# Performance work log

Measured on AMD Instinct MI355X. Metric: run time of the kernel, lower is better.

## Reference

```python
import jax, jax.numpy as jnp
import numpy as np

B, T, IN_DIM, H, W = 32, 20, 3, 1, 256
HID = 64
FC1_IN = HID * T * H * W  # 327680
FC1_OUT = 512
OUT_DIM = 3


def setup_inputs() -> dict:
    key = jax.random.key(0)
    ks = jax.random.split(key, 6)
    s = 0.02
    return dict(
        x=jax.random.normal(ks[0], (B, T, IN_DIM, H, W), dtype=jnp.float32),
        conv_w0=jax.random.normal(ks[1], (4 * HID, IN_DIM + HID, 3, 3), dtype=jnp.float32) * s,
        conv_b0=jnp.zeros((4 * HID,), dtype=jnp.float32),
        conv_w1=jax.random.normal(ks[2], (4 * HID, HID + HID, 3, 3), dtype=jnp.float32) * s,
        conv_b1=jnp.zeros((4 * HID,), dtype=jnp.float32),
        fc1_w=jax.random.normal(ks[3], (FC1_OUT, FC1_IN), dtype=jnp.float32) * s,
        fc1_b=jnp.zeros((FC1_OUT,), dtype=jnp.float32),
        fc2_w=jax.random.normal(ks[4], (OUT_DIM, FC1_OUT), dtype=jnp.float32) * s,
        fc2_b=jnp.zeros((OUT_DIM,), dtype=jnp.float32),
    )


def _convlstm_layer(inp, w, b):
    # inp: (B, T, C, H, W); w: (4*hid, C+hid, kh, kw)
    Bn, Tn, C, Hn, Wn = inp.shape
    hid = w.shape[0] // 4
    h0 = jnp.zeros((Bn, hid, Hn, Wn), inp.dtype)

    def step(carry, x_t):
        h, c = carry
        z = jnp.concatenate([x_t, h], axis=1)  # (B, C+hid, H, W)
        gates = jax.lax.conv_general_dilated(
            z, w, window_strides=(1, 1), padding='SAME',
            dimension_numbers=('NCHW', 'OIHW', 'NCHW')) + b[None, :, None, None]
        i, f, o, g = jnp.split(gates, 4, axis=1)
        c_new = jax.nn.sigmoid(f) * c + jax.nn.sigmoid(i) * jnp.tanh(g)
        h_new = jax.nn.sigmoid(o) * jnp.tanh(c_new)
        return (h_new, c_new), h_new

    _, hs = jax.lax.scan(step, (h0, h0), jnp.swapaxes(inp, 0, 1))
    return jnp.swapaxes(hs, 0, 1)  # (B, T, hid, H, W)


def reference(x, conv_w0, conv_b0, conv_w1, conv_b1, fc1_w, fc1_b, fc2_w, fc2_b):
    h = _convlstm_layer(x, conv_w0, conv_b0)
    h = _convlstm_layer(h, conv_w1, conv_b1)
    flat = h.reshape(h.shape[0], -1)  # (B, T*hid*H*W), torch .view order
    z = jax.nn.relu(flat @ fc1_w.T + fc1_b)
    out = z @ fc2_w.T + fc2_b
    return jnp.concatenate([out[:, :2], jax.nn.sigmoid(out[:, 2:])], axis=1)
```

## Files before the change

### kernel.cpp

```cpp
#include <hip/hip_runtime.h>
#include <hip/hip_bf16.h>
#include <cstddef>

#define BATCH 32
#define TSTEPS 20
#define IN_DIM 3
#define WIDTH 256
#define HID 64
#define FC1_IN 327680
#define FC1_OUT 512
#define OUT_DIM 3

#define CST 5
#define MARG 6
#define REGC 44
#define CORE 6
#define ROWS 50
#define CROWS 48

#define KSLICE 1280
#define KPHASE 640
#define NSPLIT 256

typedef _Float16 half8 __attribute__((ext_vector_type(8)));
typedef float floatx4 __attribute__((ext_vector_type(4)));

__device__ __forceinline__ float sigm(float x) {
    return 1.0f / (1.0f + __expf(-x));
}
__device__ __forceinline__ float tanh_fast(float x) {
    return 1.0f - 2.0f / (__expf(2.0f * x) + 1.0f);
}


__global__ __launch_bounds__(256) void prep_w0(
    const float* __restrict__ cw0, _Float16* __restrict__ wt0)
{
    int e = blockIdx.x * 256 + threadIdx.x;
    if (e >= 256 * 96) return;
    int co = e / 96, cip = e - co * 96;
    int ci = (cip < 64) ? (3 + cip) : (cip < 67 ? cip - 64 : -1);
    float v[3] = {0.f, 0.f, 0.f};
    if (ci >= 0) {
#pragma unroll
        for (int kw = 0; kw < 3; ++kw)
            v[kw] = cw0[(size_t)(co * 67 + ci) * 9 + 3 + kw];
    }
#pragma unroll
    for (int kw = 0; kw < 3; ++kw)
        wt0[(size_t)(kw * 256 + co) * 96 + cip] = (_Float16)v[kw];
}

__global__ __launch_bounds__(256) void prep_w1(
    const float* __restrict__ cw1, _Float16* __restrict__ wt1)
{
    int e = blockIdx.x * 256 + threadIdx.x;
    int co = e >> 7, ci = e & 127;
#pragma unroll
    for (int kw = 0; kw < 3; ++kw)
        wt1[(size_t)(kw * 256 + co) * 128 + ci] =
            (_Float16)cw1[(size_t)(co * 128 + ci) * 9 + 3 + kw];
}

__global__ __launch_bounds__(256) void prep_x(
    const float* __restrict__ x, _Float16* __restrict__ xT)
{
    int e = blockIdx.x * 256 + threadIdx.x;
    if (e >= TSTEPS * BATCH * WIDTH) return;
    int t = e / (BATCH * WIDTH);
    int rem = e - t * BATCH * WIDTH;
    int b = rem >> 8, w = rem & 255;
    half8 v = {};
#pragma unroll
    for (int ci = 0; ci < 3; ++ci)
        v[ci] = (_Float16)x[(size_t)((b * TSTEPS + t) * IN_DIM + ci) * WIDTH + w];
    *(half8*)&xT[(size_t)e * 8] = v;
}

__global__ __launch_bounds__(512) void conv_chunk(
    const _Float16* __restrict__ xT,
    const _Float16* __restrict__ wt0,
    const _Float16* __restrict__ wt1,
    const float* __restrict__ cb0,
    const float* __restrict__ cb1,
    _Float16* __restrict__ fcin,
    _Float16* __restrict__ h0g,
    _Float16* __restrict__ h1g,
    float* __restrict__ c0g,
    float* __restrict__ c1g,
    int t0, int first, int save)
{
    __shared__ __align__(16) _Float16 h0s[2][ROWS * 64];
    __shared__ __align__(16) _Float16 h1s[2][ROWS * 64];
    __shared__ __align__(16) _Float16 xs[2][ROWS * 8];
    __shared__ float c0s[CROWS * 64];
    __shared__ float c1s[CROWS * 64];
    __shared__ __align__(16) _Float16 zero16[8];

    const int b    = blockIdx.x;
    const int w0   = blockIdx.y * 32;
    const int tid  = threadIdx.x;
    const int wave = tid >> 6;
    const int ln = tid & 63;
    const int lr = ln & 15;
    const int kg = ln >> 4;

    {
        _Float16* h0f = &h0s[0][0];
        _Float16* h1f = &h1s[0][0];
        for (int i = tid; i < 2 * ROWS * 64; i += 512) { h0f[i] = (_Float16)0.0f; h1f[i] = (_Float16)0.0f; }
        for (int i = tid; i < CROWS * 64; i += 512) { c0s[i] = 0.0f; c1s[i] = 0.0f; }
        for (int i = tid; i < ROWS * 8; i += 512) xs[1][i] = (_Float16)0.0f;
        if (tid < 8) zero16[tid] = (_Float16)0.0f;
    }
    __syncthreads();

    {
        if (tid < ROWS) {
            int w = w0 - 7 + tid;
            half8 v = {};
            if (w >= 0 && w < WIDTH)
                v = *(const half8*)&xT[((size_t)(t0 * BATCH + b) * WIDTH + w) * 8];
            *(half8*)&xs[0][tid * 8] = v;
        }
        if (!first) {
            for (int i = tid; i < REGC * 8; i += 512) {
                int row = 1 + (i >> 3), c = i & 7;
                int w = w0 - 7 + row;
                half8 v0 = {}, v1 = {};
                if (w >= 0 && w < WIDTH) {
                    v0 = *(const half8*)&h0g[((size_t)b * WIDTH + w) * 64 + c * 8];
                    v1 = *(const half8*)&h1g[((size_t)b * WIDTH + w) * 64 + c * 8];
                }
                int phys = c ^ (row & 7);
                *(half8*)&h0s[1][row * 64 + phys * 8] = v0;
                *(half8*)&h1s[1][row * 64 + phys * 8] = v1;
            }
            for (int i = tid; i < REGC * 64; i += 512) {
                int n = i >> 6, hc = i & 63;
                int w = w0 - 6 + n;
                float v0 = 0.f, v1 = 0.f;
                if (w >= 0 && w < WIDTH) {
                    v0 = c0g[((size_t)b * WIDTH + w) * 64 + hc];
                    v1 = c1g[((size_t)b * WIDTH + w) * 64 + hc];
                }
                int ci = n * 64 + (hc ^ (((n >> 2) & 3) << 4));
                c0s[ci] = v0;
                c1s[ci] = v1;
            }
        }
    }

    if (wave < 4) {
        const int hc = wave * 16 + lr;

        half8 b0r[3][3][4];
#pragma unroll
        for (int kw = 0; kw < 3; ++kw)
#pragma unroll
        for (int kf = 0; kf < 3; ++kf)
#pragma unroll
        for (int cf = 0; cf < 4; ++cf)
            b0r[kw][kf][cf] = *(const half8*)&wt0[
                (size_t)(kw * 256 + cf * 64 + hc) * 96 + kf * 32 + kg * 8];

        float cbr0[4];
#pragma unroll
        for (int cf = 0; cf < 4; ++cf) cbr0[cf] = cb0[cf * 64 + hc];

        __syncthreads();

        for (int p = 0; p <= CST; ++p) {
            const int rd = (p ^ 1) & 1;
            const int wr = p & 1;
            half8 xreg = {};
            const bool xst = (p < CST - 1) && (tid < ROWS);
            if (xst) {
                int w = w0 - 7 + tid;
                if (w >= 0 && w < WIDTH)
                    xreg = *(const half8*)&xT[((size_t)((t0 + p + 1) * BATCH + b) * WIDTH + w) * 8];
            }
            if (p < CST) {
#pragma unroll
                for (int j = 0; j < 3; ++j) {
                    floatx4 acc[4];
#pragma unroll
                    for (int cf = 0; cf < 4; ++cf) acc[cf] = (floatx4)0.0f;
                    __builtin_amdgcn_s_setprio(1);
#pragma unroll
                    for (int kw = 0; kw < 3; ++kw)
#pragma unroll
                    for (int kf = 0; kf < 3; ++kf) {
                        int row = 16 * j + lr + kw;
                        half8 a;
                        if (kf < 2) {
                            int phys = (kf * 4 + kg) ^ (row & 7);
                            a = *(const half8*)&h0s[rd][row * 64 + phys * 8];
                        } else {
                            a = (kg == 0) ? *(const half8*)&xs[wr][row * 8]
                                          : *(const half8*)&zero16[0];
                        }
#pragma unroll
                        for (int cf = 0; cf < 4; ++cf)
                            acc[cf] = __builtin_amdgcn_mfma_f32_16x16x32_f16(a, b0r[kw][kf][cf], acc[cf], 0, 0, 0);
                    }
                    __builtin_amdgcn_s_setprio(0);
#pragma unroll
                    for (int r = 0; r < 4; ++r) {
                        int n = 16 * j + kg * 4 + r;
                        int cidx = n * 64 + (hc ^ (kg << 4));
                        float cv = c0s[cidx];
                        float cn = sigm(acc[1][r] + cbr0[1]) * cv
                                 + sigm(acc[0][r] + cbr0[0]) * tanh_fast(acc[3][r] + cbr0[3]);
                        c0s[cidx] = cn;
                        int w = w0 - 6 + n;
                        if (w >= 0 && w < WIDTH) {
                            _Float16 hv = (_Float16)(sigm(acc[2][r] + cbr0[2]) * tanh_fast(cn));
                            int rowo = n + 1;
                            int phys = (hc >> 3) ^ (rowo & 7);
                            *((_Float16*)((char*)&h0s[wr][0] + rowo * 128 + phys * 16 + (hc & 7) * 2)) = hv;
                        }
                    }
                }
            }
            if (xst) *(half8*)&xs[(p + 1) & 1][tid * 8] = xreg;
            __syncthreads();
        }
    } else {
        const int hc = (wave - 4) * 16 + lr;

        half8 b1r[3][4][4];
#pragma unroll
        for (int kw = 0; kw < 3; ++kw)
#pragma unroll
        for (int kf = 0; kf < 4; ++kf)
#pragma unroll
        for (int cf = 0; cf < 4; ++cf)
            b1r[kw][kf][cf] = *(const half8*)&wt1[
                (size_t)(kw * 256 + cf * 64 + hc) * 128 + kf * 32 + kg * 8];

        float cbr1[4];
#pragma unroll
        for (int cf = 0; cf < 4; ++cf) cbr1[cf] = cb1[cf * 64 + hc];

        __syncthreads();

        for (int p = 0; p <= CST; ++p) {
            const int rd   = (p ^ 1) & 1;
            const int h1rd = p & 1;
            if (p >= 1) {
#pragma unroll
                for (int j = 0; j < 3; ++j) {
                    floatx4 acc[4];
#pragma unroll
                    for (int cf = 0; cf < 4; ++cf) acc[cf] = (floatx4)0.0f;
                    __builtin_amdgcn_s_setprio(1);
#pragma unroll
                    for (int kw = 0; kw < 3; ++kw)
#pragma unroll
                    for (int kf = 0; kf < 4; ++kf) {
                        int row = 16 * j + lr + kw;
                        half8 a;
                        if (kf < 2) {
                            int phys = (kf * 4 + kg) ^ (row & 7);
                            a = *(const half8*)&h0s[rd][row * 64 + phys * 8];
                        } else {
                            int phys = ((kf - 2) * 4 + kg) ^ (row & 7);
                            a = *(const half8*)&h1s[h1rd][row * 64 + phys * 8];
                        }
#pragma unroll
                        for (int cf = 0; cf < 4; ++cf)
                            acc[cf] = __builtin_amdgcn_mfma_f32_16x16x32_f16(a, b1r[kw][kf][cf], acc[cf], 0, 0, 0);
                    }
                    __builtin_amdgcn_s_setprio(0);
#pragma unroll
                    for (int r = 0; r < 4; ++r) {
                        int n = 16 * j + kg * 4 + r;
                        int cidx = n * 64 + (hc ^ (kg << 4));
                        float cv = c1s[cidx];
                        float cn = sigm(acc[1][r] + cbr1[1]) * cv
                                 + sigm(acc[0][r] + cbr1[0]) * tanh_fast(acc[3][r] + cbr1[3]);
                        c1s[cidx] = cn;
                        _Float16 hv = (_Float16)(sigm(acc[2][r] + cbr1[2]) * tanh_fast(cn));
                        int w = w0 - 6 + n;
                        if (w >= 0 && w < WIDTH) {
                            int rowo = n + 1;
                            int phys = (hc >> 3) ^ (rowo & 7);
                            *((_Float16*)((char*)&h1s[rd][0] + rowo * 128 + phys * 16 + (hc & 7) * 2)) = hv;
                        }
                        if (n >= CORE && n < CORE + 32)
                            fcin[(size_t)b * FC1_IN + (size_t)((t0 + p - 1) * HID + hc) * WIDTH + w] = hv;
                    }
                }
            }
            __syncthreads();
        }
    }

    if (save) {
        for (int i = tid; i < 32 * 64; i += 512) {
            int n = CORE + (i >> 6);
            int hc = i & 63;
            int w = w0 + (i >> 6);
            int rowo = n + 1;
            int physh = (hc >> 3) ^ (rowo & 7);
            h0g[((size_t)b * WIDTH + w) * 64 + hc] = h0s[0][rowo * 64 + physh * 8 + (hc & 7)];
            h1g[((size_t)b * WIDTH + w) * 64 + hc] = h1s[0][rowo * 64 + physh * 8 + (hc & 7)];
            int ci = n * 64 + (hc ^ (((n >> 2) & 3) << 4));
            c0g[((size_t)b * WIDTH + w) * 64 + hc] = c0s[ci];
            c1g[((size_t)b * WIDTH + w) * 64 + hc] = c1s[ci];
        }
    }
}

__global__ __launch_bounds__(512) void fc1_mfma(
    const _Float16* __restrict__ a,
    const float* __restrict__ w,
    float* __restrict__ part)
{
    __shared__ _Float16 alds[32 * 648];

    const int blk = blockIdx.x;
    const int nh  = blockIdx.y;
    const int tid = threadIdx.x;
    const int wv  = tid >> 6;
    const int ln  = tid & 63;
    const int lg  = ln >> 4;
    const int lr  = ln & 15;
    const int k0  = blk * KSLICE;

    floatx4 acc[2][2];
#pragma unroll
    for (int bt = 0; bt < 2; ++bt)
#pragma unroll
        for (int nt = 0; nt < 2; ++nt) acc[bt][nt] = (floatx4)0.0f;

    const float* wbase[2];
#pragma unroll
    for (int nt = 0; nt < 2; ++nt)
        wbase[nt] = w + (size_t)(nh * 256 + wv * 32 + nt * 16 + lr) * FC1_IN + k0 + lg * 8;

    for (int p = 0; p < 2; ++p) {
        __syncthreads();
        for (int i = tid; i < 32 * 80; i += 512) {
            int r = i / 80;
            int c = (i - r * 80) * 8;
            *(half8*)&alds[r * 648 + c] =
                *(const half8*)&a[(size_t)r * FC1_IN + k0 + p * KPHASE + c];
        }
        __syncthreads();

        for (int kc = 0; kc < KPHASE / 32; ++kc) {
            half8 af0 = *(const half8*)&alds[lr * 648 + kc * 32 + lg * 8];
            half8 af1 = *(const half8*)&alds[(16 + lr) * 648 + kc * 32 + lg * 8];
#pragma unroll
            for (int nt = 0; nt < 2; ++nt) {
                const float* wp = wbase[nt] + p * KPHASE + kc * 32;
                float4 wlo = *(const float4*)wp;
                float4 whi = *(const float4*)(wp + 4);
                half8 bf;
                bf[0] = (_Float16)wlo.x; bf[1] = (_Float16)wlo.y;
                bf[2] = (_Float16)wlo.z; bf[3] = (_Float16)wlo.w;
                bf[4] = (_Float16)whi.x; bf[5] = (_Float16)whi.y;
                bf[6] = (_Float16)whi.z; bf[7] = (_Float16)whi.w;
                acc[0][nt] = __builtin_amdgcn_mfma_f32_16x16x32_f16(af0, bf, acc[0][nt], 0, 0, 0);
                acc[1][nt] = __builtin_amdgcn_mfma_f32_16x16x32_f16(af1, bf, acc[1][nt], 0, 0, 0);
            }
        }
    }

#pragma unroll
    for (int bt = 0; bt < 2; ++bt)
#pragma unroll
        for (int nt = 0; nt < 2; ++nt) {
            int n = nh * 256 + wv * 32 + nt * 16 + lr;
            int b = bt * 16 + lg * 4;
            *(float4*)&part[((size_t)blk * FC1_OUT + n) * BATCH + b] =
                *(float4*)&acc[bt][nt];
        }
}

__global__ __launch_bounds__(256) void fc1_reduce(
    const float* __restrict__ part, const float* __restrict__ b1,
    float* __restrict__ z1)
{
    int e = blockIdx.x * 256 + threadIdx.x;
    float s = 0.0f;
    for (int ks = 0; ks < NSPLIT; ++ks)
        s += part[(size_t)ks * (FC1_OUT * BATCH) + e];
    int n = e >> 5, b = e & 31;
    float v = s + b1[n];
    z1[(size_t)b * FC1_OUT + n] = v > 0.0f ? v : 0.0f;
}

__global__ __launch_bounds__(128) void fc2_kernel(
    const float* __restrict__ z1, const float* __restrict__ w2,
    const float* __restrict__ b2, float* __restrict__ out)
{
    int t = threadIdx.x;
    if (t >= BATCH * OUT_DIM) return;
    int b = t / OUT_DIM, n = t - b * OUT_DIM;
    const float* zr = z1 + (size_t)b * FC1_OUT;
    const float* wr = w2 + (size_t)n * FC1_OUT;
    float acc = b2[n];
    for (int k = 0; k < FC1_OUT; ++k) acc += zr[k] * wr[k];
    if (n == 2) acc = sigm(acc);
    out[(size_t)b * OUT_DIM + n] = acc;
}

extern "C" void kernel_launch(void* const* d_in, const int* in_sizes, int n_in,
                              void* d_out, int out_size, void* d_ws, size_t ws_size,
                              hipStream_t stream) {
    const float* x   = (const float*)d_in[0];
    const float* cw0 = (const float*)d_in[1];
    const float* cb0 = (const float*)d_in[2];
    const float* cw1 = (const float*)d_in[3];
    const float* cb1 = (const float*)d_in[4];
    const float* w1  = (const float*)d_in[5];
    const float* b1  = (const float*)d_in[6];
    const float* w2  = (const float*)d_in[7];
    const float* b2  = (const float*)d_in[8];
    float* out = (float*)d_out;

    const size_t S = (size_t)BATCH * WIDTH * HID;
    char* p = (char*)d_ws;
    auto alloc = [&](size_t bytes) { char* r = p; p += (bytes + 255) & ~(size_t)255; return r; };

    _Float16* wt0  = (_Float16*)alloc((size_t)3 * 256 * 96 * 2);
    _Float16* wt1  = (_Float16*)alloc((size_t)3 * 256 * 128 * 2);
    _Float16* xT   = (_Float16*)alloc((size_t)TSTEPS * BATCH * WIDTH * 8 * 2);
    _Float16* fcin = (_Float16*)alloc((size_t)BATCH * FC1_IN * 2);
    _Float16* h0g  = (_Float16*)alloc(S * 2);
    _Float16* h1g  = (_Float16*)alloc(S * 2);
    float*    c0g  = (float*)alloc(S * 4);
    float*    c1g  = (float*)alloc(S * 4);
    float*    part = (float*)alloc((size_t)NSPLIT * FC1_OUT * BATCH * 4);
    float*    z1   = (float*)alloc((size_t)BATCH * FC1_OUT * 4);

    prep_w0<<<96, 256, 0, stream>>>(cw0, wt0);
    prep_w1<<<128, 256, 0, stream>>>(cw1, wt1);
    prep_x<<<(TSTEPS * BATCH * WIDTH + 255) / 256, 256, 0, stream>>>(x, xT);

    for (int k = 0; k < 4; ++k) {
        conv_chunk<<<dim3(BATCH, 8), 512, 0, stream>>>(
            xT, wt0, wt1, cb0, cb1, fcin, h0g, h1g, c0g, c1g,
            k * CST, (k == 0) ? 1 : 0, (k < 3) ? 1 : 0);
    }

    fc1_mfma<<<dim3(NSPLIT, 2), 512, 0, stream>>>(fcin, w1, part);
    fc1_reduce<<<64, 256, 0, stream>>>(part, b1, z1);
    fc2_kernel<<<1, 128, 0, stream>>>(z1, w2, b2, out);
}
```

Before: 432.2 us.

## Convert fc1 weights to fp16 inside the latency-bound ConvLSTM kernel

The recurrent conv kernel is latency-bound, so its waves now also stream the 640 MB fp32 fc1 weight and write it out as fp16, software-pipelining the loads across timestep phases. fc1 then reads half-size fp16 weights and covers all 512 outputs per block, so the activation tile is loaded once instead of twice. The cost is extra register pressure and memory traffic inside the conv kernel, which could slow the recurrence, plus a 320 MB scratch buffer.

```diff
diff --git a/kernel.cpp b/kernel.cpp
--- a/kernel.cpp
+++ b/kernel.cpp
@@ -22,7 +22,11 @@
 #define KPHASE 640
 #define NSPLIT 256
 
+#define NF4 41943040ULL
+#define BLKF4 7168
+
 typedef _Float16 half8 __attribute__((ext_vector_type(8)));
+typedef _Float16 half4 __attribute__((ext_vector_type(4)));
 typedef float floatx4 __attribute__((ext_vector_type(4)));
 
 __device__ __forceinline__ float sigm(float x) {
@@ -88,6 +92,8 @@
     _Float16* __restrict__ h1g,
     float* __restrict__ c0g,
     float* __restrict__ c1g,
+    const float* __restrict__ w1,
+    _Float16* __restrict__ w1h,
     int t0, int first, int save)
 {
     __shared__ __align__(16) _Float16 h0s[2][ROWS * 64];
@@ -99,11 +105,14 @@
 
     const int b    = blockIdx.x;
     const int w0   = blockIdx.y * 32;
+    const int bid  = blockIdx.y * 32 + blockIdx.x;
+    const int kk   = t0 / CST;
     const int tid  = threadIdx.x;
     const int wave = tid >> 6;
     const int ln = tid & 63;
     const int lr = ln & 15;
     const int kg = ln >> 4;
+    const float4* w1v = (const float4*)w1;
 
     {
         _Float16* h0f = &h0s[0][0];
@@ -168,11 +177,35 @@
 #pragma unroll
         for (int cf = 0; cf < 4; ++cf) cbr0[cf] = cb0[cf * 64 + hc];
 
+        float4 cbuf[12];
+        size_t hbase = 0;
+
         __syncthreads();
 
         for (int p = 0; p <= CST; ++p) {
             const int rd = (p ^ 1) & 1;
             const int wr = p & 1;
+            const size_t rbase = ((size_t)(kk * 6 + p) * 256 + bid) * BLKF4;
+
+            if (p > 0) {
+#pragma unroll
+                for (int i = 0; i < 12; ++i) {
+                    size_t idx = hbase + (size_t)i * 64 + ln;
+                    if (idx < NF4) {
+                        half4 hv4;
+                        hv4[0] = (_Float16)cbuf[i].x; hv4[1] = (_Float16)cbuf[i].y;
+                        hv4[2] = (_Float16)cbuf[i].z; hv4[3] = (_Float16)cbuf[i].w;
+                        *(half4*)&w1h[idx * 4] = hv4;
+                    }
+                }
+            }
+            const size_t abase = rbase + (size_t)(wave * 2 + 0) * 768;
+#pragma unroll
+            for (int i = 0; i < 12; ++i) {
+                size_t idx = abase + (size_t)i * 64 + ln;
+                cbuf[i] = (idx < NF4) ? w1v[idx] : float4{0.f, 0.f, 0.f, 0.f};
+            }
+
             half8 xreg = {};
             const bool xst = (p < CST - 1) && (tid < ROWS);
             if (xst) {
@@ -223,8 +256,34 @@
                     }
                 }
             }
+#pragma unroll
+            for (int i = 0; i < 12; ++i) {
+                size_t idx = abase + (size_t)i * 64 + ln;
+                if (idx < NF4) {
+                    half4 hv4;
+                    hv4[0] = (_Float16)cbuf[i].x; hv4[1] = (_Float16)cbuf[i].y;
+                    hv4[2] = (_Float16)cbuf[i].z; hv4[3] = (_Float16)cbuf[i].w;
+                    *(half4*)&w1h[idx * 4] = hv4;
+                }
+            }
+            hbase = rbase + (size_t)(wave * 2 + 1) * 768;
+#pragma unroll
+            for (int i = 0; i < 12; ++i) {
+                size_t idx = hbase + (size_t)i * 64 + ln;
+                cbuf[i] = (idx < NF4) ? w1v[idx] : float4{0.f, 0.f, 0.f, 0.f};
+            }
             if (xst) *(half8*)&xs[(p + 1) & 1][tid * 8] = xreg;
             __syncthreads();
+        }
+#pragma unroll
+        for (int i = 0; i < 12; ++i) {
+            size_t idx = hbase + (size_t)i * 64 + ln;
+            if (idx < NF4) {
+                half4 hv4;
+                hv4[0] = (_Float16)cbuf[i].x; hv4[1] = (_Float16)cbuf[i].y;
+                hv4[2] = (_Float16)cbuf[i].z; hv4[3] = (_Float16)cbuf[i].w;
+                *(half4*)&w1h[idx * 4] = hv4;
+            }
         }
     } else {
         const int hc = (wave - 4) * 16 + lr;
@@ -243,11 +302,35 @@
 #pragma unroll
         for (int cf = 0; cf < 4; ++cf) cbr1[cf] = cb1[cf * 64 + hc];
 
+        float4 dbuf[2];
+        size_t hbase = 0;
+
         __syncthreads();
 
         for (int p = 0; p <= CST; ++p) {
             const int rd   = (p ^ 1) & 1;
             const int h1rd = p & 1;
+            const size_t rbase = ((size_t)(kk * 6 + p) * 256 + bid) * BLKF4;
+
+            if (p > 0) {
+#pragma unroll
+                for (int i = 0; i < 2; ++i) {
+                    size_t idx = hbase + (size_t)i * 64 + ln;
+                    if (idx < NF4) {
+                        half4 hv4;
+                        hv4[0] = (_Float16)dbuf[i].x; hv4[1] = (_Float16)dbuf[i].y;
+                        hv4[2] = (_Float16)dbuf[i].z; hv4[3] = (_Float16)dbuf[i].w;
+                        *(half4*)&w1h[idx * 4] = hv4;
+                    }
+                }
+            }
+            const size_t abase = rbase + 6144 + (size_t)((wave - 4) * 2 + 0) * 128;
+#pragma unroll
+            for (int i = 0; i < 2; ++i) {
+                size_t idx = abase + (size_t)i * 64 + ln;
+                dbuf[i] = (idx < NF4) ? w1v[idx] : float4{0.f, 0.f, 0.f, 0.f};
+            }
+
             if (p >= 1) {
 #pragma unroll
                 for (int j = 0; j < 3; ++j) {
@@ -293,7 +376,33 @@
                     }
                 }
             }
+#pragma unroll
+            for (int i = 0; i < 2; ++i) {
+                size_t idx = abase + (size_t)i * 64 + ln;
+                if (idx < NF4) {
+                    half4 hv4;
+                    hv4[0] = (_Float16)dbuf[i].x; hv4[1] = (_Float16)dbuf[i].y;
+                    hv4[2] = (_Float16)dbuf[i].z; hv4[3] = (_Float16)dbuf[i].w;
+                    *(half4*)&w1h[idx * 4] = hv4;
+                }
+            }
+            hbase = rbase + 6144 + (size_t)((wave - 4) * 2 + 1) * 128;
+#pragma unroll
+            for (int i = 0; i < 2; ++i) {
+                size_t idx = hbase + (size_t)i * 64 + ln;
+                dbuf[i] = (idx < NF4) ? w1v[idx] : float4{0.f, 0.f, 0.f, 0.f};
+            }
             __syncthreads();
+        }
+#pragma unroll
+        for (int i = 0; i < 2; ++i) {
+            size_t idx = hbase + (size_t)i * 64 + ln;
+            if (idx < NF4) {
+                half4 hv4;
+                hv4[0] = (_Float16)dbuf[i].x; hv4[1] = (_Float16)dbuf[i].y;
+                hv4[2] = (_Float16)dbuf[i].z; hv4[3] = (_Float16)dbuf[i].w;
+                *(half4*)&w1h[idx * 4] = hv4;
+            }
         }
     }
 
@@ -315,13 +424,12 @@
 
 __global__ __launch_bounds__(512) void fc1_mfma(
     const _Float16* __restrict__ a,
-    const float* __restrict__ w,
+    const _Float16* __restrict__ wh,
     float* __restrict__ part)
 {
     __shared__ _Float16 alds[32 * 648];
 
     const int blk = blockIdx.x;
-    const int nh  = blockIdx.y;
     const int tid = threadIdx.x;
     const int wv  = tid >> 6;
     const int ln  = tid & 63;
@@ -329,16 +437,16 @@
     const int lr  = ln & 15;
     const int k0  = blk * KSLICE;
 
-    floatx4 acc[2][2];
+    floatx4 acc[2][4];
 #pragma unroll
     for (int bt = 0; bt < 2; ++bt)
 #pragma unroll
-        for (int nt = 0; nt < 2; ++nt) acc[bt][nt] = (floatx4)0.0f;
-
-    const float* wbase[2];
-#pragma unroll
-    for (int nt = 0; nt < 2; ++nt)
-        wbase[nt] = w + (size_t)(nh * 256 + wv * 32 + nt * 16 + lr) * FC1_IN + k0 + lg * 8;
+        for (int nt = 0; nt < 4; ++nt) acc[bt][nt] = (floatx4)0.0f;
+
+    const _Float16* wbase[4];
+#pragma unroll
+    for (int nt = 0; nt < 4; ++nt)
+        wbase[nt] = wh + (size_t)(wv * 64 + nt * 16 + lr) * FC1_IN + k0 + lg * 8;
 
     for (int p = 0; p < 2; ++p) {
         __syncthreads();
@@ -354,15 +462,8 @@
             half8 af0 = *(const half8*)&alds[lr * 648 + kc * 32 + lg * 8];
             half8 af1 = *(const half8*)&alds[(16 + lr) * 648 + kc * 32 + lg * 8];
 #pragma unroll
-            for (int nt = 0; nt < 2; ++nt) {
-                const float* wp = wbase[nt] + p * KPHASE + kc * 32;
-                float4 wlo = *(const float4*)wp;
-                float4 whi = *(const float4*)(wp + 4);
-                half8 bf;
-                bf[0] = (_Float16)wlo.x; bf[1] = (_Float16)wlo.y;
-                bf[2] = (_Float16)wlo.z; bf[3] = (_Float16)wlo.w;
-                bf[4] = (_Float16)whi.x; bf[5] = (_Float16)whi.y;
-                bf[6] = (_Float16)whi.z; bf[7] = (_Float16)whi.w;
+            for (int nt = 0; nt < 4; ++nt) {
+                half8 bf = *(const half8*)(wbase[nt] + p * KPHASE + kc * 32);
                 acc[0][nt] = __builtin_amdgcn_mfma_f32_16x16x32_f16(af0, bf, acc[0][nt], 0, 0, 0);
                 acc[1][nt] = __builtin_amdgcn_mfma_f32_16x16x32_f16(af1, bf, acc[1][nt], 0, 0, 0);
             }
@@ -372,8 +473,8 @@
 #pragma unroll
     for (int bt = 0; bt < 2; ++bt)
 #pragma unroll
-        for (int nt = 0; nt < 2; ++nt) {
-            int n = nh * 256 + wv * 32 + nt * 16 + lr;
+        for (int nt = 0; nt < 4; ++nt) {
+            int n = wv * 64 + nt * 16 + lr;
             int b = bt * 16 + lg * 4;
             *(float4*)&part[((size_t)blk * FC1_OUT + n) * BATCH + b] =
                 *(float4*)&acc[bt][nt];
@@ -436,6 +537,7 @@
     float*    c1g  = (float*)alloc(S * 4);
     float*    part = (float*)alloc((size_t)NSPLIT * FC1_OUT * BATCH * 4);
     float*    z1   = (float*)alloc((size_t)BATCH * FC1_OUT * 4);
+    _Float16* w1h  = (_Float16*)alloc((size_t)FC1_OUT * FC1_IN * 2);
 
     prep_w0<<<96, 256, 0, stream>>>(cw0, wt0);
     prep_w1<<<128, 256, 0, stream>>>(cw1, wt1);
@@ -444,10 +546,11 @@
     for (int k = 0; k < 4; ++k) {
         conv_chunk<<<dim3(BATCH, 8), 512, 0, stream>>>(
             xT, wt0, wt1, cb0, cb1, fcin, h0g, h1g, c0g, c1g,
+            w1, w1h,
             k * CST, (k == 0) ? 1 : 0, (k < 3) ? 1 : 0);
     }
 
-    fc1_mfma<<<dim3(NSPLIT, 2), 512, 0, stream>>>(fcin, w1, part);
+    fc1_mfma<<<NSPLIT, 512, 0, stream>>>(fcin, w1h, part);
     fc1_reduce<<<64, 256, 0, stream>>>(part, b1, z1);
     fc2_kernel<<<1, 128, 0, stream>>>(z1, w2, b2, out);
 }
```

Measured after the change: 778.3 us. +80.1%, slower.
